# Kernel tuning notes

Measured on AMD Instinct MI355X. Metric: run time of the kernel, lower is better.

The kernel has to match this reference:

```python
import jax, jax.numpy as jnp
import numpy as np

K = 32
EPS = 1e-5  # BatchNorm eps; eval mode with running_mean=0, running_var=1


def knn_idx(x):
    # x: [B, C, N] -> idx of K nearest neighbors [B, N, K]
    inner = -2.0 * jnp.einsum('bcn,bcm->bnm', x, x)
    xx = jnp.sum(x * x, axis=1)  # [B, N]
    pd = -xx[:, :, None] - inner - xx[:, None, :]  # negative squared dist
    return jax.lax.top_k(pd, K)[1]


def get_neighbors(x):
    # x: [B, C, N] -> edge features [B, N, K, 2C] (nbr - ctr, ctr)
    idx = knn_idx(x)
    xt = jnp.transpose(x, (0, 2, 1))  # [B, N, C]
    nbrs = jax.vmap(lambda p, i: p[i])(xt, idx)  # [B, N, K, C]
    ctr = jnp.broadcast_to(xt[:, :, None, :], nbrs.shape)
    return jnp.concatenate([nbrs - ctr, ctr], axis=-1)


def bn_eval(h, g, b, nd):
    # inference-mode BN, running_mean=0, running_var=1
    shape = [1, -1] + [1] * (nd - 2)
    return h * (g / jnp.sqrt(1.0 + EPS)).reshape(shape) + b.reshape(shape)


def edge_conv(x, W, g, b):
    # x: [B, C, N] -> [B, O, N]; 1x1 conv over edge feats + BN + LeakyReLU + max over K
    feat = get_neighbors(x)  # [B, N, K, 2C]
    h = jnp.einsum('bnkc,oc->bonk', feat, W)
    h = jax.nn.leaky_relu(bn_eval(h, g, b, 4), 0.2)
    return jnp.max(h, axis=-1)


def setup_inputs():
    key = jax.random.key(0)
    ks = jax.random.split(key, 40)
    B, N = 4, 2048

    def rn(i, shape, s=0.1):
        return jax.random.normal(ks[i], shape, jnp.float32) * s

    def gm(i, c):
        return 1.0 + rn(i, (c,))

    inp = {
        'x': jax.random.normal(ks[0], (B, 3, N), jnp.float32),
        'l': jax.random.normal(ks[1], (B, 5), jnp.float32),
        'n': jax.random.normal(ks[2], (B, 7), jnp.float32),
        'W1': rn(3, (64, 6)), 'g1': gm(4, 64), 'b1': rn(5, (64,)),
        'W2': rn(6, (64, 128)), 'g2': gm(7, 64), 'b2': rn(8, (64,)),
        'W3': rn(9, (128, 128)), 'g3': gm(10, 128), 'b3': rn(11, (128,)),
        'W4': rn(12, (256, 256)), 'g4': gm(13, 256), 'b4': rn(14, (256,)),
        'W5': rn(15, (1024, 512)), 'g5': gm(16, 1024), 'b5': rn(17, (1024,)),
        'W6': rn(18, (64, 5)), 'g6': gm(19, 64), 'b6': rn(20, (64,)),
        'W7': rn(21, (64, 7)), 'g7': gm(22, 64), 'b7': rn(23, (64,)),
        'L1': rn(24, (512, 1152)), 'g8': gm(25, 512), 'b8': rn(26, (512,)),
        'L2': rn(27, (256, 512)), 'L2b': rn(28, (256,)), 'g9': gm(29, 256), 'b9': rn(30, (256,)),
        'L3': rn(31, (28, 256)), 'L3b': rn(32, (28,)),
    }
    return inp


def reference(x, l, n, W1, g1, b1, W2, g2, b2, W3, g3, b3, W4, g4, b4,
              W5, g5, b5, W6, g6, b6, W7, g7, b7,
              L1, g8, b8, L2, L2b, g9, b9, L3, L3b):
    x1 = edge_conv(x, W1, g1, b1)    # [B, 64, N]
    x2 = edge_conv(x1, W2, g2, b2)   # [B, 64, N]
    x3 = edge_conv(x2, W3, g3, b3)   # [B, 128, N]
    x4 = edge_conv(x3, W4, g4, b4)   # [B, 256, N]
    cat = jnp.concatenate([x1, x2, x3, x4], axis=1)  # [B, 512, N]
    h = jnp.einsum('bcn,oc->bon', cat, W5)
    h = jax.nn.leaky_relu(bn_eval(h, g5, b5, 3), 0.2)
    h = jnp.max(h, axis=-1)  # global max pool -> [B, 1024]
    lf = jax.nn.leaky_relu(bn_eval(jnp.einsum('bc,oc->bo', l, W6), g6, b6, 2), 0.2)
    nf = jax.nn.leaky_relu(bn_eval(jnp.einsum('bc,oc->bo', n, W7), g7, b7, 2), 0.2)
    v = jnp.concatenate([h, lf, nf], axis=-1)  # [B, 1152]
    v = jax.nn.relu(bn_eval(v @ L1.T, g8, b8, 2))  # dropout = identity (eval)
    v = jax.nn.relu(bn_eval(v @ L2.T + L2b, g9, b9, 2))
    return v @ L3.T + L3b  # [B, 28]
```

## Files before the change

### kernel.cpp

```cpp
#include <hip/hip_runtime.h>
#include <hip/hip_bf16.h>

#define NPTS 2048
#define NB 4
#define KNN 32
#define NIN 33

static __device__ __forceinline__ float b2f(__hip_bfloat16 v) { return __bfloat162float(v); }
#define ISQ 0.99999499996875f

typedef __attribute__((ext_vector_type(8))) short short8v;
typedef __attribute__((ext_vector_type(4))) float f32x4;

static __device__ __forceinline__ unsigned ordkey(float f) {
  unsigned u = __float_as_uint(f);
  return u ^ (unsigned)(((int)u >> 31) | 0x80000000);
}

static __device__ __forceinline__ void loadv(const float* p, float (&d)[1]) { d[0] = *p; }
static __device__ __forceinline__ void loadv(const float* p, float (&d)[2]) {
  float2 v = *(const float2*)p; d[0] = v.x; d[1] = v.y;
}
static __device__ __forceinline__ void loadv(const float* p, float (&d)[4]) {
  float4 v = *(const float4*)p; d[0] = v.x; d[1] = v.y; d[2] = v.z; d[3] = v.w;
}

static __device__ __forceinline__ float wave_red_sum(float s) {
#pragma unroll
  for (int off = 32; off > 0; off >>= 1) s += __shfl_xor(s, off);
  return s;
}

__global__ __launch_bounds__(64) void detect_kernel(const unsigned short* __restrict__ x,
                                                    int* __restrict__ flag) {
  int cnt = 0;
  for (int i = threadIdx.x; i < 512; i += 64) {
    unsigned e = (x[i] >> 7) & 0xFFu;
    if (e >= 0xC6u) cnt++;
  }
#pragma unroll
  for (int off = 32; off > 0; off >>= 1) cnt += __shfl_down(cnt, off);
  if (threadIdx.x == 0) flag[0] = (cnt == 0) ? 1 : 0;
}

struct CvtArgs {
  const void* src[NIN];
  int off[NIN + 1];
};

__global__ __launch_bounds__(256) void cvt_all_kernel(CvtArgs a, float* __restrict__ out,
                                                      int total, int nb1,
                                                      __hip_bfloat16* __restrict__ w5bf,
                                                      float* __restrict__ xxb,
                                                      const int* __restrict__ flag) {
  int fl = flag[0];
  if ((int)blockIdx.x < nb1) {
    int t = blockIdx.x * 256 + threadIdx.x;
    if (t >= total) return;
    int s = 0;
    while (t >= a.off[s + 1]) s++;
    int j = t - a.off[s];
    float v;
    if (fl) v = b2f(((const __hip_bfloat16*)a.src[s])[j]);
    else    v = ((const float*)a.src[s])[j];
    out[t] = v;
  } else if ((int)blockIdx.x < nb1 + 2048) {
    int t = (blockIdx.x - nb1) * 256 + threadIdx.x;
    if (fl) w5bf[t] = ((const __hip_bfloat16*)a.src[15])[t];
    else    w5bf[t] = __float2bfloat16(((const float*)a.src[15])[t]);
  } else {
    int t = (blockIdx.x - nb1 - 2048) * 256 + threadIdx.x;
    int b = t >> 11, m = t & 2047;
    float s = 0.f;
#pragma unroll
    for (int c = 0; c < 3; ++c) {
      long o = ((long)b * 3 + c) * NPTS + m;
      float v = fl ? b2f(((const __hip_bfloat16*)a.src[0])[o])
                   : ((const float*)a.src[0])[o];
      s = fmaf(v, v, s);
    }
    xxb[t] = s;
  }
}

template <int C>
static __device__ __forceinline__ void pd_body(char* smem, const float* __restrict__ x,
                                               long bstride, const float* __restrict__ xx,
                                               unsigned* __restrict__ keys, int t, int bb) {
  constexpr int KT = (C < 16) ? C : 16;
  float* At = (float*)smem;
  float* Bt = At + KT * 64;
  unsigned* Ts = (unsigned*)(Bt + KT * 64);
  int tj = (int)((sqrtf(8.f * (float)t + 1.f) - 1.f) * 0.5f);
  while ((tj + 1) * (tj + 2) / 2 <= t) tj++;
  while (tj * (tj + 1) / 2 > t) tj--;
  int ti = t - tj * (tj + 1) / 2;
  int n0 = ti * 64, m0 = tj * 64;
  int tid = threadIdx.x, tx = tid & 15, ty = tid >> 4;
  const float* xb = x + (long)bb * bstride;
  float acc[4][4] = {};
  for (int k0 = 0; k0 < C; k0 += KT) {
    for (int lin = tid; lin < KT * 64; lin += 256) {
      int r = lin >> 6, col = lin & 63;
      At[r * 64 + col] = xb[(long)(k0 + r) * NPTS + n0 + col];
      Bt[r * 64 + col] = xb[(long)(k0 + r) * NPTS + m0 + col];
    }
    __syncthreads();
#pragma unroll
    for (int kc = 0; kc < KT; ++kc) {
      float4 av = *(const float4*)&At[kc * 64 + ty * 4];
      float4 bv = *(const float4*)&Bt[kc * 64 + tx * 4];
      acc[0][0] = fmaf(av.x, bv.x, acc[0][0]); acc[0][1] = fmaf(av.x, bv.y, acc[0][1]);
      acc[0][2] = fmaf(av.x, bv.z, acc[0][2]); acc[0][3] = fmaf(av.x, bv.w, acc[0][3]);
      acc[1][0] = fmaf(av.y, bv.x, acc[1][0]); acc[1][1] = fmaf(av.y, bv.y, acc[1][1]);
      acc[1][2] = fmaf(av.y, bv.z, acc[1][2]); acc[1][3] = fmaf(av.y, bv.w, acc[1][3]);
      acc[2][0] = fmaf(av.z, bv.x, acc[2][0]); acc[2][1] = fmaf(av.z, bv.y, acc[2][1]);
      acc[2][2] = fmaf(av.z, bv.z, acc[2][2]); acc[2][3] = fmaf(av.z, bv.w, acc[2][3]);
      acc[3][0] = fmaf(av.w, bv.x, acc[3][0]); acc[3][1] = fmaf(av.w, bv.y, acc[3][1]);
      acc[3][2] = fmaf(av.w, bv.z, acc[3][2]); acc[3][3] = fmaf(av.w, bv.w, acc[3][3]);
    }
    __syncthreads();
  }
  const float* xxq = xx + (long)bb * NPTS;
  float4 xxm = *(const float4*)&xxq[m0 + tx * 4];
  unsigned* kb = keys + ((long)bb << 22);
  unsigned ok[4][4];
#pragma unroll
  for (int i = 0; i < 4; ++i) {
    float xxn = xxq[n0 + ty * 4 + i];
    ok[i][0] = ordkey((-xxn - (-2.f * acc[i][0])) - xxm.x);
    ok[i][1] = ordkey((-xxn - (-2.f * acc[i][1])) - xxm.y);
    ok[i][2] = ordkey((-xxn - (-2.f * acc[i][2])) - xxm.z);
    ok[i][3] = ordkey((-xxn - (-2.f * acc[i][3])) - xxm.w);
    uint4 o = make_uint4(ok[i][0], ok[i][1], ok[i][2], ok[i][3]);
    *(uint4*)&kb[(long)(n0 + ty * 4 + i) * NPTS + m0 + tx * 4] = o;
  }
  if (ti != tj) {
#pragma unroll
    for (int i = 0; i < 4; ++i)
#pragma unroll
      for (int j = 0; j < 4; ++j) Ts[(tx * 4 + j) * 68 + ty * 4 + i] = ok[i][j];
    __syncthreads();
#pragma unroll
    for (int i = 0; i < 4; ++i)
      *(uint4*)&kb[(long)(m0 + ty * 4 + i) * NPTS + n0 + tx * 4] =
          *(const uint4*)&Ts[(ty * 4 + i) * 68 + tx * 4];
  }
}

template <int C>
static __device__ __forceinline__ void yzt_body(char* smem, const float* __restrict__ x,
                                                long bstride, const float* __restrict__ W, int O,
                                                float* __restrict__ yt, float* __restrict__ zt,
                                                int b, int m0, int o0) {
  constexpr int KT = (C < 16) ? C : 16;
  float* Xs = (float*)smem;
  float* Wy = Xs + KT * 64;
  float* Wp = Wy + KT * 64;
  int tid = threadIdx.x, tx = tid & 15, ty = tid >> 4;
  const float* xb = x + (long)b * bstride;
  const int twoC = 2 * C;
  float accy[4][4] = {}, accp[4][4] = {};
  for (int k0 = 0; k0 < C; k0 += KT) {
    for (int lin = tid; lin < KT * 64; lin += 256) {
      int r = lin >> 6, col = lin & 63;
      Xs[r * 64 + col] = xb[(long)(k0 + r) * NPTS + m0 + col];
      float wy = W[(o0 + col) * twoC + k0 + r];
      Wy[r * 64 + col] = wy;
      Wp[r * 64 + col] = W[(o0 + col) * twoC + C + k0 + r] - wy;
    }
    __syncthreads();
#pragma unroll
    for (int kc = 0; kc < KT; ++kc) {
      float4 wv = *(const float4*)&Wy[kc * 64 + tx * 4];
      float4 pv = *(const float4*)&Wp[kc * 64 + tx * 4];
      float xm[4];
      xm[0] = Xs[kc * 64 + ty * 4 + 0]; xm[1] = Xs[kc * 64 + ty * 4 + 1];
      xm[2] = Xs[kc * 64 + ty * 4 + 2]; xm[3] = Xs[kc * 64 + ty * 4 + 3];
#pragma unroll
      for (int i = 0; i < 4; ++i) {
        accy[i][0] = fmaf(xm[i], wv.x, accy[i][0]);
        accy[i][1] = fmaf(xm[i], wv.y, accy[i][1]);
        accy[i][2] = fmaf(xm[i], wv.z, accy[i][2]);
        accy[i][3] = fmaf(xm[i], wv.w, accy[i][3]);
        accp[i][0] = fmaf(xm[i], pv.x, accp[i][0]);
        accp[i][1] = fmaf(xm[i], pv.y, accp[i][1]);
        accp[i][2] = fmaf(xm[i], pv.z, accp[i][2]);
        accp[i][3] = fmaf(xm[i], pv.w, accp[i][3]);
      }
    }
    __syncthreads();
  }
#pragma unroll
  for (int i = 0; i < 4; ++i) {
    long base = ((long)b * NPTS + m0 + ty * 4 + i) * O + o0 + tx * 4;
    *(float4*)&yt[base] = make_float4(accy[i][0], accy[i][1], accy[i][2], accy[i][3]);
    *(float4*)&zt[base] = make_float4(accp[i][0], accp[i][1], accp[i][2], accp[i][3]);
  }
}

template <int C, int O64>
__global__ __launch_bounds__(256) void pdyzt_kernel(const float* __restrict__ x, long bstride,
                                                    const float* __restrict__ xx,
                                                    unsigned* __restrict__ keys,
                                                    const float* __restrict__ W,
                                                    float* __restrict__ yt,
                                                    float* __restrict__ zt, int npd) {
  constexpr int KT = (C < 16) ? C : 16;
  constexpr size_t S1 = (size_t)KT * 64 * 2 * 4 + 64 * 68 * 4;
  constexpr size_t S2 = (size_t)KT * 64 * 3 * 4;
  constexpr size_t SM = S1 > S2 ? S1 : S2;
  __shared__ __align__(16) char smem[SM];
  int bid = blockIdx.x;
  if (bid < npd) {
    int bb = bid % NB, t = bid / NB;
    pd_body<C>(smem, x, bstride, xx, keys, t, bb);
  } else {
    int rem = bid - npd;
    int b = rem % NB; rem /= NB;
    int m0 = (rem % 32) * 64; rem /= 32;
    int o0 = rem * 64;
    yzt_body<C>(smem, x, bstride, W, O64 * 64, yt, zt, b, m0, o0);
  }
}

__global__ __launch_bounds__(256) void select_kernel(const unsigned* __restrict__ keys,
                                                     int* __restrict__ idxout) {
  int wave = threadIdx.x >> 6, lane = threadIdx.x & 63;
  int q = blockIdx.x * 4 + wave;
  int bloc = q >> 11, n = q & 2047;
  const uint4* rp = (const uint4*)(keys + ((long)((bloc << 11) | n) << 11));
  unsigned K[32];
#pragma unroll
  for (int t = 0; t < 8; ++t) {
    uint4 kk = rp[t * 64 + lane];
    K[4 * t + 0] = kk.x; K[4 * t + 1] = kk.y; K[4 * t + 2] = kk.z; K[4 * t + 3] = kk.w;
  }
  unsigned t0 = 0, t1 = 0, t2 = 0, t3 = 0;
#pragma unroll
  for (int s = 0; s < 32; ++s) {
    unsigned k = K[s];
    if (k > t3) {
      if (k > t1) {
        if (k > t0) { t3 = t2; t2 = t1; t1 = t0; t0 = k; }
        else        { t3 = t2; t2 = t1; t1 = k; }
      } else {
        if (k > t2) { t3 = t2; t2 = k; }
        else        { t3 = k; }
      }
    }
  }
  unsigned orv = t0 | t1 | t2 | t3, andv = t0 & t1 & t2 & t3;
#pragma unroll
  for (int xm = 32; xm >= 1; xm >>= 1) {
    orv  |= __shfl_xor(orv, xm);
    andv &= __shfl_xor(andv, xm);
  }
  unsigned V = orv ^ andv;
  unsigned P = andv & ~V;
  int need = KNN;
  for (int b = 31; b >= 0; --b) {
    unsigned bit = 1u << b;
    if (!(V & bit)) continue;
    unsigned hm = 0xFFFFFFFFu << b;
    unsigned Pb = (P & hm) | bit;
    int c = (int)__popcll(__ballot((t0 & hm) == Pb)) +
            (int)__popcll(__ballot((t1 & hm) == Pb)) +
            (int)__popcll(__ballot((t2 & hm) == Pb)) +
            (int)__popcll(__ballot((t3 & hm) == Pb));
    if (c >= need) P |= bit;
    else need -= c;
  }
  int cg = 0;
#pragma unroll
  for (int s = 0; s < 32; ++s) cg += (int)__popcll(__ballot(K[s] > P));
  if (cg > KNN - 1) {
    unsigned orf = K[0], anf = K[0];
#pragma unroll
    for (int s = 1; s < 32; ++s) { orf |= K[s]; anf &= K[s]; }
#pragma unroll
    for (int xm = 32; xm >= 1; xm >>= 1) {
      orf |= __shfl_xor(orf, xm);
      anf &= __shfl_xor(anf, xm);
    }
    unsigned Vf = orf ^ anf;
    P = anf & ~Vf;
    need = KNN;
    for (int b = 31; b >= 0; --b) {
      unsigned bit = 1u << b;
      if (!(Vf & bit)) continue;
      unsigned hm = 0xFFFFFFFFu << b;
      unsigned Pb = (P & hm) | bit;
      int c = 0;
#pragma unroll
      for (int s = 0; s < 32; ++s) c += (int)__popcll(__ballot((K[s] & hm) == Pb));
      if (c >= need) P |= bit;
      else need -= c;
    }
  }
  int* orow = idxout + ((bloc << 11) | n) * KNN;
  int base = 0;
  unsigned eqmask = 0;
#pragma unroll
  for (int s = 0; s < 32; ++s) {
    bool take = K[s] > P;
    unsigned long long bal = __ballot(take);
    if (take) {
      int pos = base + (int)__popcll(bal & ((1ull << lane) - 1ull));
      orow[pos] = ((s >> 2) << 8) + lane * 4 + (s & 3);
    }
    base += (int)__popcll(bal);
    if (K[s] == P) eqmask |= (1u << s);
  }
  int rem = KNN - base;
  for (int it = 0; it < rem; ++it) {
    unsigned mym = 0xFFFFFFFFu;
    if (eqmask) {
      int s = __ffs(eqmask) - 1;
      mym = (unsigned)(((s >> 2) << 8) + lane * 4 + (s & 3));
    }
    unsigned wm = mym;
#pragma unroll
    for (int xm = 32; xm >= 1; xm >>= 1) {
      unsigned o = __shfl_xor(wm, xm);
      wm = o < wm ? o : wm;
    }
    if (mym == wm) {
      orow[base + it] = (int)wm;
      eqmask &= eqmask - 1;
    }
  }
}

template <int C>
__global__ __launch_bounds__(256) void pdgemmsym_kernel(const float* __restrict__ x, long bstride,
                                                        const float* __restrict__ xx,
                                                        unsigned* __restrict__ keys) {
  constexpr int KT = (C < 16) ? C : 16;
  constexpr size_t SM = (size_t)KT * 64 * 2 * 4 + 64 * 68 * 4;
  __shared__ __align__(16) char smem[SM];
  pd_body<C>(smem, x, bstride, xx, keys, blockIdx.x, blockIdx.y);
}

template <int C>
__global__ __launch_bounds__(256) void yzt_kernel(const float* __restrict__ x, long bstride,
                                                  const float* __restrict__ W, int O,
                                                  float* __restrict__ yt, float* __restrict__ zt) {
  constexpr int KT = (C < 16) ? C : 16;
  constexpr size_t SM = (size_t)KT * 64 * 3 * 4;
  __shared__ __align__(16) char smem[SM];
  yzt_body<C>(smem, x, bstride, W, O, yt, zt, blockIdx.z, blockIdx.y * 64, blockIdx.x * 64);
}

template <int RO>
__global__ __launch_bounds__(256) void gmaxt_kernel(const float* __restrict__ yt,
                                                    const float* __restrict__ zt,
                                                    const int* __restrict__ idx,
                                                    const float* __restrict__ g,
                                                    const float* __restrict__ bb,
                                                    float* __restrict__ out, long obstride,
                                                    float* __restrict__ xxout,
                                                    __hip_bfloat16* __restrict__ catbf, int loff) {
  constexpr int O = RO * 64;
  int wave = threadIdx.x >> 6, lane = threadIdx.x & 63;
  int n = blockIdx.x * 4 + wave, b = blockIdx.y;
  int jreg = idx[((b << 11) + n) * KNN + (lane & 31)];
  int obase = lane * RO;
  float gs[RO], bs[RO], zr[RO], acc[RO];
  loadv(zt + ((long)(b << 11) + n) * O + obase, zr);
#pragma unroll
  for (int r = 0; r < RO; ++r) {
    gs[r] = g[obase + r] * ISQ;
    bs[r] = bb[obase + r];
    acc[r] = -INFINITY;
  }
  const float* yb = yt + ((long)(b << 11)) * O + obase;
#pragma unroll
  for (int k = 0; k < KNN; ++k) {
    int j = __shfl(jreg, k);
    float yv[RO];
    loadv(yb + (long)j * O, yv);
#pragma unroll
    for (int r = 0; r < RO; ++r) {
      float v = fmaf(gs[r], yv[r] + zr[r], bs[r]);
      v = v >= 0.f ? v : 0.2f * v;
      acc[r] = fmaxf(acc[r], v);
    }
  }
  float* op = out + (long)b * obstride + (long)obase * NPTS + n;
#pragma unroll
  for (int r = 0; r < RO; ++r) op[(long)r * NPTS] = acc[r];
  __hip_bfloat16* cb = catbf + ((long)(b << 11) + n) * 512 + loff + obase;
#pragma unroll
  for (int r = 0; r < RO; ++r) cb[r] = __float2bfloat16(acc[r]);
  if (xxout) {
    float ss = 0.f;
#pragma unroll
    for (int r = 0; r < RO; ++r) ss = fmaf(acc[r], acc[r], ss);
    ss = wave_red_sum(ss);
    if (lane == 0) xxout[(b << 11) + n] = ss;
  }
}

__global__ __launch_bounds__(256) void gemm5m_kernel(const __hip_bfloat16* __restrict__ catbf,
                                                     const __hip_bfloat16* __restrict__ w5bf,
                                                     const float* __restrict__ g5,
                                                     const float* __restrict__ b5,
                                                     float* __restrict__ pmax) {
  __shared__ __align__(16) short Bs[2][8 * 64 * 8];
  int b = blockIdx.z, po0 = blockIdx.y * 128, n0 = blockIdx.x * 64;
  int wave = threadIdx.x >> 6, lane = threadIdx.x & 63;
  int quad = lane >> 4, l15 = lane & 15;
  const short* cbase = (const short*)catbf + ((long)(b << 11) + n0) * 512;
  const short* abase0 = (const short*)w5bf + (long)(po0 + wave * 32 + l15) * 512 + quad * 8;
  const short* abase1 = abase0 + 16 * 512;
  const short* bsrc0 = cbase + (long)lane * 512 + (2 * wave + 0) * 8;
  const short* bsrc1 = cbase + (long)lane * 512 + (2 * wave + 1) * 8;
  short* bdst0 = &Bs[0][((2 * wave + 0) * 64 + lane) * 8];
  short* bdst1 = &Bs[0][((2 * wave + 1) * 64 + lane) * 8];
  const int bufstride = 8 * 64 * 8;

  short8v Br[2][2], Ar[2][2][2];
  f32x4 acc[2][4] = {};

  Br[0][0] = *(const short8v*)(bsrc0);
  Br[0][1] = *(const short8v*)(bsrc1);
#pragma unroll
  for (int h = 0; h < 2; ++h)
#pragma unroll
    for (int j = 0; j < 2; ++j)
      Ar[0][h][j] = *(const short8v*)((h ? abase1 : abase0) + j * 32);
  *(short8v*)bdst0 = Br[0][0];
  *(short8v*)bdst1 = Br[0][1];
  Br[1][0] = *(const short8v*)(bsrc0 + 64);
  Br[1][1] = *(const short8v*)(bsrc1 + 64);
#pragma unroll
  for (int h = 0; h < 2; ++h)
#pragma unroll
    for (int j = 0; j < 2; ++j)
      Ar[1][h][j] = *(const short8v*)((h ? abase1 : abase0) + 64 + j * 32);
  __syncthreads();

  for (int it = 0; it < 8; ++it) {
    int cur = it & 1;
    const short* lb = &Bs[cur][0];
#pragma unroll
    for (int j = 0; j < 2; ++j) {
#pragma unroll
      for (int nt = 0; nt < 4; ++nt) {
        short8v bf = *(const short8v*)(lb + ((j * 4 + quad) * 64 + nt * 16 + l15) * 8);
        acc[0][nt] = __builtin_amdgcn_mfma_f32_16x16x32_bf16(Ar[cur][0][j], bf, acc[0][nt], 0, 0, 0);
        acc[1][nt] = __builtin_amdgcn_mfma_f32_16x16x32_bf16(Ar[cur][1][j], bf, acc[1][nt], 0, 0, 0);
      }
    }
    if (it < 7) {
      if (it < 6) {
        int ks = (it + 2) * 64;
        Br[cur][0] = *(const short8v*)(bsrc0 + ks);
        Br[cur][1] = *(const short8v*)(bsrc1 + ks);
#pragma unroll
        for (int h = 0; h < 2; ++h)
#pragma unroll
          for (int j = 0; j < 2; ++j)
            Ar[cur][h][j] = *(const short8v*)((h ? abase1 : abase0) + ks + j * 32);
      }
      int nb = cur ^ 1;
      *(short8v*)(bdst0 + nb * bufstride) = Br[nb][0];
      *(short8v*)(bdst1 + nb * bufstride) = Br[nb][1];
      __syncthreads();
    }
  }

#pragma unroll
  for (int h = 0; h < 2; ++h) {
#pragma unroll
    for (int r = 0; r < 4; ++r) {
      int po = po0 + wave * 32 + h * 16 + quad * 4 + r;
      float sc = g5[po] * ISQ;
      float bi = b5[po];
      float mx = -INFINITY;
#pragma unroll
      for (int nt = 0; nt < 4; ++nt) {
        float v = fmaf(sc, acc[h][nt][r], bi);
        v = v >= 0.f ? v : 0.2f * v;
        mx = fmaxf(mx, v);
      }
#pragma unroll
      for (int xm = 1; xm < 16; xm <<= 1) mx = fmaxf(mx, __shfl_xor(mx, xm));
      if (l15 == 0) pmax[(long)(b * 1024 + po) * 32 + blockIdx.x] = mx;
    }
  }
}

__global__ __launch_bounds__(256) void redlfnf_kernel(const float* __restrict__ pmax,
                                                      const float* __restrict__ l,
                                                      const float* __restrict__ nn,
                                                      const float* __restrict__ W6,
                                                      const float* __restrict__ g6,
                                                      const float* __restrict__ b6,
                                                      const float* __restrict__ W7,
                                                      const float* __restrict__ g7,
                                                      const float* __restrict__ b7,
                                                      float* __restrict__ v) {
  if (blockIdx.x < 16) {
    int t = blockIdx.x * 256 + threadIdx.x;
    float mx = -INFINITY;
#pragma unroll
    for (int j = 0; j < 32; ++j) mx = fmaxf(mx, pmax[(long)t * 32 + j]);
    int b = t >> 10, po = t & 1023;
    v[b * 1152 + po] = mx;
  } else {
    int idx = (blockIdx.x - 16) * 256 + threadIdx.x;
    int b = idx >> 7, t = idx & 127;
    if (t < 64) {
      float s = 0.f;
#pragma unroll
      for (int c = 0; c < 5; ++c) s = fmaf(W6[t * 5 + c], l[b * 5 + c], s);
      float val = fmaf(g6[t] * ISQ, s, b6[t]);
      v[b * 1152 + 1024 + t] = val >= 0.f ? val : 0.2f * val;
    } else {
      int o = t - 64;
      float s = 0.f;
#pragma unroll
      for (int c = 0; c < 7; ++c) s = fmaf(W7[o * 7 + c], nn[b * 7 + c], s);
      float val = fmaf(g7[o] * ISQ, s, b7[o]);
      v[b * 1152 + 1088 + o] = val >= 0.f ? val : 0.2f * val;
    }
  }
}

__global__ __launch_bounds__(256) void head1_kernel(const float* __restrict__ v,
                                                    const float* __restrict__ L1,
                                                    const float* __restrict__ g8,
                                                    const float* __restrict__ b8,
                                                    float* __restrict__ v1) {
  int wave = threadIdx.x >> 6, lane = threadIdx.x & 63;
  int t = blockIdx.x * 4 + wave;
  int b = t >> 9, o = t & 511;
  const float* vb = v + b * 1152;
  const float* wr = L1 + (long)o * 1152;
  float s = 0.f;
#pragma unroll
  for (int c = lane; c < 1152; c += 64) s = fmaf(wr[c], vb[c], s);
  s = wave_red_sum(s);
  if (lane == 0) {
    float val = fmaf(g8[o] * ISQ, s, b8[o]);
    v1[t] = fmaxf(val, 0.f);
  }
}

__global__ __launch_bounds__(256) void head2_kernel(const float* __restrict__ v1,
                                                    const float* __restrict__ L2,
                                                    const float* __restrict__ L2b,
                                                    const float* __restrict__ g9,
                                                    const float* __restrict__ b9,
                                                    float* __restrict__ v2) {
  int wave = threadIdx.x >> 6, lane = threadIdx.x & 63;
  int t = blockIdx.x * 4 + wave;
  int b = t >> 8, o = t & 255;
  const float* vb = v1 + b * 512;
  const float* wr = L2 + (long)o * 512;
  float s = 0.f;
#pragma unroll
  for (int c = lane; c < 512; c += 64) s = fmaf(wr[c], vb[c], s);
  s = wave_red_sum(s);
  if (lane == 0) {
    float sv = s + L2b[o];
    float val = fmaf(g9[o] * ISQ, sv, b9[o]);
    v2[t] = fmaxf(val, 0.f);
  }
}

__global__ __launch_bounds__(256) void head3_kernel(const float* __restrict__ v2,
                                                    const float* __restrict__ L3,
                                                    const float* __restrict__ L3b,
                                                    void* __restrict__ out,
                                                    const int* __restrict__ flag) {
  int wave = threadIdx.x >> 6, lane = threadIdx.x & 63;
  int t = blockIdx.x * 4 + wave;
  if (t >= 112) return;
  int b = t / 28, o = t % 28;
  const float* vb = v2 + b * 256;
  const float* wr = L3 + o * 256;
  float s = 0.f;
#pragma unroll
  for (int c = lane; c < 256; c += 64) s = fmaf(wr[c], vb[c], s);
  s = wave_red_sum(s);
  if (lane == 0) {
    float sv = s + L3b[o];
    if (flag[0]) ((__hip_bfloat16*)out)[t] = __float2bfloat16(sv);
    else         ((float*)out)[t] = sv;
  }
}

extern "C" void kernel_launch(void* const* d_in, const int* in_sizes, int n_in,
                              void* d_out, int out_size, void* d_ws, size_t ws_size,
                              hipStream_t stream) {
  CvtArgs ca;
  int off[NIN + 1];
  off[0] = 0;
  for (int i = 0; i < NIN; ++i) {
    ca.src[i] = d_in[i];
    off[i + 1] = off[i] + in_sizes[i];
    ca.off[i] = off[i];
  }
  ca.off[NIN] = off[NIN];
  const int total = off[NIN];

  int* flag = (int*)d_ws;
  float* fin = (float*)((char*)d_ws + 64);
  const float* xf  = fin + off[0];
  const float* lf  = fin + off[1];
  const float* nf  = fin + off[2];
  const float* W1f = fin + off[3];  const float* g1f = fin + off[4];  const float* b1f = fin + off[5];
  const float* W2f = fin + off[6];  const float* g2f = fin + off[7];  const float* b2f_ = fin + off[8];
  const float* W3f = fin + off[9];  const float* g3f = fin + off[10]; const float* b3f = fin + off[11];
  const float* W4f = fin + off[12]; const float* g4f = fin + off[13]; const float* b4f = fin + off[14];
  const float* g5f = fin + off[16]; const float* b5f = fin + off[17];
  const float* W6f = fin + off[18]; const float* g6f = fin + off[19]; const float* b6f = fin + off[20];
  const float* W7f = fin + off[21]; const float* g7f = fin + off[22]; const float* b7f = fin + off[23];
  const float* L1f = fin + off[24]; const float* g8f = fin + off[25]; const float* b8f = fin + off[26];
  const float* L2f = fin + off[27]; const float* L2bf = fin + off[28];
  const float* g9f = fin + off[29]; const float* b9f = fin + off[30];
  const float* L3f = fin + off[31]; const float* L3bf = fin + off[32];

  float* p = fin + ((total + 15) & ~15);
  float* cat  = p;
  float* yb   = cat + 4 * 512 * NPTS;
  float* zb   = yb + 4 * 256 * NPTS;
  float* xxb  = zb + 4 * 256 * NPTS;
  int*   idxb = (int*)(xxb + 4 * NPTS);
  float* pmax = (float*)(idxb + 4 * NPTS * KNN);
  float* vb   = pmax + 4 * 1024 * 32;
  float* v1b  = vb + 4 * 1152;
  float* v2b  = v1b + 4 * 512;
  __hip_bfloat16* w5bf  = (__hip_bfloat16*)(v2b + 4 * 256);
  __hip_bfloat16* catbf = w5bf + 1024 * 512;
  unsigned* keys_tail = (unsigned*)(catbf + (size_t)4 * NPTS * 512);

  size_t need_full = (size_t)((char*)(keys_tail + (size_t)NB * NPTS * NPTS) - (char*)d_ws);
  int bpass = (ws_size >= need_full) ? NB : 1;
  unsigned* keys = (bpass == NB) ? keys_tail : (unsigned*)yb;

  const long bst1 = 3L * NPTS;
  const long bstc = 512L * NPTS;
  const int NTRI = 32 * 33 / 2;
  const int NPD = NTRI * NB;
  const int nb1 = (total + 255) / 256;

  detect_kernel<<<1, 64, 0, stream>>>((const unsigned short*)d_in[0], flag);
  cvt_all_kernel<<<nb1 + 2048 + 32, 256, 0, stream>>>(ca, fin, total, nb1, w5bf, xxb, flag);

  if (bpass == NB) {
    pdyzt_kernel<3, 1><<<NPD + 1 * 32 * NB, 256, 0, stream>>>(xf, bst1, xxb, keys, W1f, yb, zb, NPD);
    select_kernel<<<512 * NB, 256, 0, stream>>>(keys, idxb);
  } else {
    for (int b0 = 0; b0 < NB; b0 += bpass) {
      pdgemmsym_kernel<3><<<dim3(NTRI, bpass), 256, 0, stream>>>(xf + b0 * bst1, bst1, xxb + b0 * NPTS, keys);
      select_kernel<<<512 * bpass, 256, 0, stream>>>(keys, idxb + (long)b0 * NPTS * KNN);
    }
    yzt_kernel<3><<<dim3(1, 32, NB), 256, 0, stream>>>(xf, bst1, W1f, 64, yb, zb);
  }
  gmaxt_kernel<1><<<dim3(512, NB), 256, 0, stream>>>(yb, zb, idxb, g1f, b1f, cat, bstc, xxb, catbf, 0);

  if (bpass == NB) {
    pdyzt_kernel<64, 1><<<NPD + 1 * 32 * NB, 256, 0, stream>>>(cat, bstc, xxb, keys, W2f, yb, zb, NPD);
    select_kernel<<<512 * NB, 256, 0, stream>>>(keys, idxb);
  } else {
    for (int b0 = 0; b0 < NB; b0 += bpass) {
      pdgemmsym_kernel<64><<<dim3(NTRI, bpass), 256, 0, stream>>>(cat + b0 * bstc, bstc, xxb + b0 * NPTS, keys);
      select_kernel<<<512 * bpass, 256, 0, stream>>>(keys, idxb + (long)b0 * NPTS * KNN);
    }
    yzt_kernel<64><<<dim3(1, 32, NB), 256, 0, stream>>>(cat, bstc, W2f, 64, yb, zb);
  }
  gmaxt_kernel<1><<<dim3(512, NB), 256, 0, stream>>>(yb, zb, idxb, g2f, b2f_, cat + 64L * NPTS, bstc, xxb, catbf, 64);

  if (bpass == NB) {
    pdyzt_kernel<64, 2><<<NPD + 2 * 32 * NB, 256, 0, stream>>>(cat + 64L * NPTS, bstc, xxb, keys, W3f, yb, zb, NPD);
    select_kernel<<<512 * NB, 256, 0, stream>>>(keys, idxb);
  } else {
    for (int b0 = 0; b0 < NB; b0 += bpass) {
      pdgemmsym_kernel<64><<<dim3(NTRI, bpass), 256, 0, stream>>>(cat + 64L * NPTS + b0 * bstc, bstc, xxb + b0 * NPTS, keys);
      select_kernel<<<512 * bpass, 256, 0, stream>>>(keys, idxb + (long)b0 * NPTS * KNN);
    }
    yzt_kernel<64><<<dim3(2, 32, NB), 256, 0, stream>>>(cat + 64L * NPTS, bstc, W3f, 128, yb, zb);
  }
  gmaxt_kernel<2><<<dim3(512, NB), 256, 0, stream>>>(yb, zb, idxb, g3f, b3f, cat + 128L * NPTS, bstc, xxb, catbf, 128);

  if (bpass == NB) {
    pdyzt_kernel<128, 4><<<NPD + 4 * 32 * NB, 256, 0, stream>>>(cat + 128L * NPTS, bstc, xxb, keys, W4f, yb, zb, NPD);
    select_kernel<<<512 * NB, 256, 0, stream>>>(keys, idxb);
  } else {
    for (int b0 = 0; b0 < NB; b0 += bpass) {
      pdgemmsym_kernel<128><<<dim3(NTRI, bpass), 256, 0, stream>>>(cat + 128L * NPTS + b0 * bstc, bstc, xxb + b0 * NPTS, keys);
      select_kernel<<<512 * bpass, 256, 0, stream>>>(keys, idxb + (long)b0 * NPTS * KNN);
    }
    yzt_kernel<128><<<dim3(4, 32, NB), 256, 0, stream>>>(cat + 128L * NPTS, bstc, W4f, 256, yb, zb);
  }
  gmaxt_kernel<4><<<dim3(512, NB), 256, 0, stream>>>(yb, zb, idxb, g4f, b4f, cat + 256L * NPTS, bstc, (float*)nullptr, catbf, 256);

  gemm5m_kernel<<<dim3(32, 8, NB), 256, 0, stream>>>(catbf, w5bf, g5f, b5f, pmax);
  redlfnf_kernel<<<18, 256, 0, stream>>>(pmax, lf, nf, W6f, g6f, b6f, W7f, g7f, b7f, vb);

  head1_kernel<<<512, 256, 0, stream>>>(vb, L1f, g8f, b8f, v1b);
  head2_kernel<<<256, 256, 0, stream>>>(v1b, L2f, L2bf, g9f, b9f, v2b);
  head3_kernel<<<28, 256, 0, stream>>>(v2b, L3f, L3bf, d_out, flag);
}
```

Baseline: 545.4 us.

## Fuse 3-channel kNN distance with top-k selection and co-schedule yzt with select

For the first layer (3 input channels), a new knn3 kernel computes pairwise distances directly in registers from shared-memory coordinates and selects the top-32 in the same wave. This avoids writing and re-reading the 2048x2048 key matrix. For the later layers, the yzt projection GEMM blocks move from the pairwise-distance kernel into the select kernel, so distance and select become separate launches with the projection overlapped alongside selection. The shared selection code is factored into a templated helper that supports two index layouts. Tie-breaking order may differ because the first layer uses a different index mapping.

```diff
diff --git a/kernel.cpp b/kernel.cpp
--- a/kernel.cpp
+++ b/kernel.cpp
@@ -83,6 +83,137 @@
   }
 }
 
+template <int MODE>
+static __device__ __forceinline__ int midx(int s, int lane) {
+  return MODE == 0 ? (((s >> 2) << 8) + lane * 4 + (s & 3)) : (s * 64 + lane);
+}
+
+template <int MODE>
+static __device__ __forceinline__ void select_from_K(unsigned (&K)[32], int lane,
+                                                     int* __restrict__ orow) {
+  unsigned t0 = 0, t1 = 0, t2 = 0, t3 = 0;
+#pragma unroll
+  for (int s = 0; s < 32; ++s) {
+    unsigned k = K[s];
+    if (k > t3) {
+      if (k > t1) {
+        if (k > t0) { t3 = t2; t2 = t1; t1 = t0; t0 = k; }
+        else        { t3 = t2; t2 = t1; t1 = k; }
+      } else {
+        if (k > t2) { t3 = t2; t2 = k; }
+        else        { t3 = k; }
+      }
+    }
+  }
+  unsigned orv = t0 | t1 | t2 | t3, andv = t0 & t1 & t2 & t3;
+#pragma unroll
+  for (int xm = 32; xm >= 1; xm >>= 1) {
+    orv  |= __shfl_xor(orv, xm);
+    andv &= __shfl_xor(andv, xm);
+  }
+  unsigned V = orv ^ andv;
+  unsigned P = andv & ~V;
+  int need = KNN;
+  for (int b = 31; b >= 0; --b) {
+    unsigned bit = 1u << b;
+    if (!(V & bit)) continue;
+    unsigned hm = 0xFFFFFFFFu << b;
+    unsigned Pb = (P & hm) | bit;
+    int c = (int)__popcll(__ballot((t0 & hm) == Pb)) +
+            (int)__popcll(__ballot((t1 & hm) == Pb)) +
+            (int)__popcll(__ballot((t2 & hm) == Pb)) +
+            (int)__popcll(__ballot((t3 & hm) == Pb));
+    if (c >= need) P |= bit;
+    else need -= c;
+  }
+  int cg = 0;
+#pragma unroll
+  for (int s = 0; s < 32; ++s) cg += (int)__popcll(__ballot(K[s] > P));
+  if (cg > KNN - 1) {
+    unsigned orf = K[0], anf = K[0];
+#pragma unroll
+    for (int s = 1; s < 32; ++s) { orf |= K[s]; anf &= K[s]; }
+#pragma unroll
+    for (int xm = 32; xm >= 1; xm >>= 1) {
+      orf |= __shfl_xor(orf, xm);
+      anf &= __shfl_xor(anf, xm);
+    }
+    unsigned Vf = orf ^ anf;
+    P = anf & ~Vf;
+    need = KNN;
+    for (int b = 31; b >= 0; --b) {
+      unsigned bit = 1u << b;
+      if (!(Vf & bit)) continue;
+      unsigned hm = 0xFFFFFFFFu << b;
+      unsigned Pb = (P & hm) | bit;
+      int c = 0;
+#pragma unroll
+      for (int s = 0; s < 32; ++s) c += (int)__popcll(__ballot((K[s] & hm) == Pb));
+      if (c >= need) P |= bit;
+      else need -= c;
+    }
+  }
+  int base = 0;
+  unsigned eqmask = 0;
+#pragma unroll
+  for (int s = 0; s < 32; ++s) {
+    bool take = K[s] > P;
+    unsigned long long bal = __ballot(take);
+    if (take) {
+      int pos = base + (int)__popcll(bal & ((1ull << lane) - 1ull));
+      orow[pos] = midx<MODE>(s, lane);
+    }
+    base += (int)__popcll(bal);
+    if (K[s] == P) eqmask |= (1u << s);
+  }
+  int rem = KNN - base;
+  for (int it = 0; it < rem; ++it) {
+    unsigned mym = 0xFFFFFFFFu;
+    if (eqmask) {
+      int s = __ffs(eqmask) - 1;
+      mym = (unsigned)midx<MODE>(s, lane);
+    }
+    unsigned wm = mym;
+#pragma unroll
+    for (int xm = 32; xm >= 1; xm >>= 1) {
+      unsigned o = __shfl_xor(wm, xm);
+      wm = o < wm ? o : wm;
+    }
+    if (mym == wm) {
+      orow[base + it] = (int)wm;
+      eqmask &= eqmask - 1;
+    }
+  }
+}
+
+__global__ __launch_bounds__(256) void knn3_kernel(const float* __restrict__ xf,
+                                                   const float* __restrict__ xxb,
+                                                   int* __restrict__ idxout) {
+  __shared__ float xs[3 * NPTS];
+  __shared__ float xxs[NPTS];
+  int b = blockIdx.y;
+  int tid = threadIdx.x, wave = tid >> 6, lane = tid & 63;
+  const float* xb = xf + (long)b * 3 * NPTS;
+  for (int i = tid; i < 3 * NPTS; i += 256) xs[i] = xb[i];
+  for (int i = tid; i < NPTS; i += 256) xxs[i] = xxb[(b << 11) + i];
+  __syncthreads();
+  int n = blockIdx.x * 4 + wave;
+  float q0 = xs[n], q1 = xs[NPTS + n], q2 = xs[2 * NPTS + n];
+  float xxn = xxs[n];
+  unsigned K[32];
+#pragma unroll
+  for (int s = 0; s < 32; ++s) {
+    int m = s * 64 + lane;
+    float d = 0.f;
+    d = fmaf(q0, xs[m], d);
+    d = fmaf(q1, xs[NPTS + m], d);
+    d = fmaf(q2, xs[2 * NPTS + m], d);
+    float pdv = (-xxn - (-2.f * d)) - xxs[m];
+    K[s] = ordkey(pdv);
+  }
+  select_from_K<1>(K, lane, idxout + (((b << 11) | n) * KNN));
+}
+
 template <int C>
 static __device__ __forceinline__ void pd_body(char* smem, const float* __restrict__ x,
                                                long bstride, const float* __restrict__ xx,
@@ -199,24 +330,34 @@
   }
 }
 
+static __device__ __forceinline__ void select_body(const unsigned* __restrict__ keys,
+                                                   int* __restrict__ idxout, int q) {
+  int lane = threadIdx.x & 63;
+  int bloc = q >> 11, n = q & 2047;
+  const uint4* rp = (const uint4*)(keys + ((long)((bloc << 11) | n) << 11));
+  unsigned K[32];
+#pragma unroll
+  for (int t = 0; t < 8; ++t) {
+    uint4 kk = rp[t * 64 + lane];
+    K[4 * t + 0] = kk.x; K[4 * t + 1] = kk.y; K[4 * t + 2] = kk.z; K[4 * t + 3] = kk.w;
+  }
+  select_from_K<0>(K, lane, idxout + ((bloc << 11) | n) * KNN);
+}
+
 template <int C, int O64>
-__global__ __launch_bounds__(256) void pdyzt_kernel(const float* __restrict__ x, long bstride,
-                                                    const float* __restrict__ xx,
-                                                    unsigned* __restrict__ keys,
-                                                    const float* __restrict__ W,
-                                                    float* __restrict__ yt,
-                                                    float* __restrict__ zt, int npd) {
+__global__ __launch_bounds__(256) void selyzt_kernel(const unsigned* __restrict__ keys,
+                                                     int* __restrict__ idxout,
+                                                     const float* __restrict__ x, long bstride,
+                                                     const float* __restrict__ W,
+                                                     float* __restrict__ yt,
+                                                     float* __restrict__ zt, int nsel) {
   constexpr int KT = (C < 16) ? C : 16;
-  constexpr size_t S1 = (size_t)KT * 64 * 2 * 4 + 64 * 68 * 4;
-  constexpr size_t S2 = (size_t)KT * 64 * 3 * 4;
-  constexpr size_t SM = S1 > S2 ? S1 : S2;
-  __shared__ __align__(16) char smem[SM];
-  int bid = blockIdx.x;
-  if (bid < npd) {
-    int bb = bid % NB, t = bid / NB;
-    pd_body<C>(smem, x, bstride, xx, keys, t, bb);
+  __shared__ __align__(16) char smem[(size_t)KT * 64 * 3 * 4];
+  if ((int)blockIdx.x < nsel) {
+    int wave = threadIdx.x >> 6;
+    select_body(keys, idxout, blockIdx.x * 4 + wave);
   } else {
-    int rem = bid - npd;
+    int rem = blockIdx.x - nsel;
     int b = rem % NB; rem /= NB;
     int m0 = (rem % 32) * 64; rem /= 32;
     int o0 = rem * 64;
@@ -226,110 +367,8 @@
 
 __global__ __launch_bounds__(256) void select_kernel(const unsigned* __restrict__ keys,
                                                      int* __restrict__ idxout) {
-  int wave = threadIdx.x >> 6, lane = threadIdx.x & 63;
-  int q = blockIdx.x * 4 + wave;
-  int bloc = q >> 11, n = q & 2047;
-  const uint4* rp = (const uint4*)(keys + ((long)((bloc << 11) | n) << 11));
-  unsigned K[32];
-#pragma unroll
-  for (int t = 0; t < 8; ++t) {
-    uint4 kk = rp[t * 64 + lane];
-    K[4 * t + 0] = kk.x; K[4 * t + 1] = kk.y; K[4 * t + 2] = kk.z; K[4 * t + 3] = kk.w;
-  }
-  unsigned t0 = 0, t1 = 0, t2 = 0, t3 = 0;
-#pragma unroll
-  for (int s = 0; s < 32; ++s) {
-    unsigned k = K[s];
-    if (k > t3) {
-      if (k > t1) {
-        if (k > t0) { t3 = t2; t2 = t1; t1 = t0; t0 = k; }
-        else        { t3 = t2; t2 = t1; t1 = k; }
-      } else {
-        if (k > t2) { t3 = t2; t2 = k; }
-        else        { t3 = k; }
-      }
-    }
-  }
-  unsigned orv = t0 | t1 | t2 | t3, andv = t0 & t1 & t2 & t3;
-#pragma unroll
-  for (int xm = 32; xm >= 1; xm >>= 1) {
-    orv  |= __shfl_xor(orv, xm);
-    andv &= __shfl_xor(andv, xm);
-  }
-  unsigned V = orv ^ andv;
-  unsigned P = andv & ~V;
-  int need = KNN;
-  for (int b = 31; b >= 0; --b) {
-    unsigned bit = 1u << b;
-    if (!(V & bit)) continue;
-    unsigned hm = 0xFFFFFFFFu << b;
-    unsigned Pb = (P & hm) | bit;
-    int c = (int)__popcll(__ballot((t0 & hm) == Pb)) +
-            (int)__popcll(__ballot((t1 & hm) == Pb)) +
-            (int)__popcll(__ballot((t2 & hm) == Pb)) +
-            (int)__popcll(__ballot((t3 & hm) == Pb));
-    if (c >= need) P |= bit;
-    else need -= c;
-  }
-  int cg = 0;
-#pragma unroll
-  for (int s = 0; s < 32; ++s) cg += (int)__popcll(__ballot(K[s] > P));
-  if (cg > KNN - 1) {
-    unsigned orf = K[0], anf = K[0];
-#pragma unroll
-    for (int s = 1; s < 32; ++s) { orf |= K[s]; anf &= K[s]; }
-#pragma unroll
-    for (int xm = 32; xm >= 1; xm >>= 1) {
-      orf |= __shfl_xor(orf, xm);
-      anf &= __shfl_xor(anf, xm);
-    }
-    unsigned Vf = orf ^ anf;
-    P = anf & ~Vf;
-    need = KNN;
-    for (int b = 31; b >= 0; --b) {
-      unsigned bit = 1u << b;
-      if (!(Vf & bit)) continue;
-      unsigned hm = 0xFFFFFFFFu << b;
-      unsigned Pb = (P & hm) | bit;
-      int c = 0;
-#pragma unroll
-      for (int s = 0; s < 32; ++s) c += (int)__popcll(__ballot((K[s] & hm) == Pb));
-      if (c >= need) P |= bit;
-      else need -= c;
-    }
-  }
-  int* orow = idxout + ((bloc << 11) | n) * KNN;
-  int base = 0;
-  unsigned eqmask = 0;
-#pragma unroll
-  for (int s = 0; s < 32; ++s) {
-    bool take = K[s] > P;
-    unsigned long long bal = __ballot(take);
-    if (take) {
-      int pos = base + (int)__popcll(bal & ((1ull << lane) - 1ull));
-      orow[pos] = ((s >> 2) << 8) + lane * 4 + (s & 3);
-    }
-    base += (int)__popcll(bal);
-    if (K[s] == P) eqmask |= (1u << s);
-  }
-  int rem = KNN - base;
-  for (int it = 0; it < rem; ++it) {
-    unsigned mym = 0xFFFFFFFFu;
-    if (eqmask) {
-      int s = __ffs(eqmask) - 1;
-      mym = (unsigned)(((s >> 2) << 8) + lane * 4 + (s & 3));
-    }
-    unsigned wm = mym;
-#pragma unroll
-    for (int xm = 32; xm >= 1; xm >>= 1) {
-      unsigned o = __shfl_xor(wm, xm);
-      wm = o < wm ? o : wm;
-    }
-    if (mym == wm) {
-      orow[base + it] = (int)wm;
-      eqmask &= eqmask - 1;
-    }
-  }
+  int wave = threadIdx.x >> 6;
+  select_body(keys, idxout, blockIdx.x * 4 + wave);
 }
 
 template <int C>
@@ -645,27 +684,19 @@
   const long bst1 = 3L * NPTS;
   const long bstc = 512L * NPTS;
   const int NTRI = 32 * 33 / 2;
-  const int NPD = NTRI * NB;
   const int nb1 = (total + 255) / 256;
+  const int NSEL = NB * 512;
 
   detect_kernel<<<1, 64, 0, stream>>>((const unsigned short*)d_in[0], flag);
   cvt_all_kernel<<<nb1 + 2048 + 32, 256, 0, stream>>>(ca, fin, total, nb1, w5bf, xxb, flag);
 
+  knn3_kernel<<<dim3(512, NB), 256, 0, stream>>>(xf, xxb, idxb);
+  yzt_kernel<3><<<dim3(1, 32, NB), 256, 0, stream>>>(xf, bst1, W1f, 64, yb, zb);
+  gmaxt_kernel<1><<<dim3(512, NB), 256, 0, stream>>>(yb, zb, idxb, g1f, b1f, cat, bstc, xxb, catbf, 0);
+
   if (bpass == NB) {
-    pdyzt_kernel<3, 1><<<NPD + 1 * 32 * NB, 256, 0, stream>>>(xf, bst1, xxb, keys, W1f, yb, zb, NPD);
-    select_kernel<<<512 * NB, 256, 0, stream>>>(keys, idxb);
-  } else {
-    for (int b0 = 0; b0 < NB; b0 += bpass) {
-      pdgemmsym_kernel<3><<<dim3(NTRI, bpass), 256, 0, stream>>>(xf + b0 * bst1, bst1, xxb + b0 * NPTS, keys);
-      select_kernel<<<512 * bpass, 256, 0, stream>>>(keys, idxb + (long)b0 * NPTS * KNN);
-    }
-    yzt_kernel<3><<<dim3(1, 32, NB), 256, 0, stream>>>(xf, bst1, W1f, 64, yb, zb);
-  }
-  gmaxt_kernel<1><<<dim3(512, NB), 256, 0, stream>>>(yb, zb, idxb, g1f, b1f, cat, bstc, xxb, catbf, 0);
-
-  if (bpass == NB) {
-    pdyzt_kernel<64, 1><<<NPD + 1 * 32 * NB, 256, 0, stream>>>(cat, bstc, xxb, keys, W2f, yb, zb, NPD);
-    select_kernel<<<512 * NB, 256, 0, stream>>>(keys, idxb);
+    pdgemmsym_kernel<64><<<dim3(NTRI, NB), 256, 0, stream>>>(cat, bstc, xxb, keys);
+    selyzt_kernel<64, 1><<<NSEL + 1 * 32 * NB, 256, 0, stream>>>(keys, idxb, cat, bstc, W2f, yb, zb, NSEL);
   } else {
     for (int b0 = 0; b0 < NB; b0 += bpass) {
       pdgemmsym_kernel<64><<<dim3(NTRI, bpass), 256, 0, stream>>>(cat + b0 * bstc, bstc, xxb + b0 * NPTS, keys);
@@ -676,8 +707,8 @@
   gmaxt_kernel<1><<<dim3(512, NB), 256, 0, stream>>>(yb, zb, idxb, g2f, b2f_, cat + 64L * NPTS, bstc, xxb, catbf, 64);
 
   if (bpass == NB) {
-    pdyzt_kernel<64, 2><<<NPD + 2 * 32 * NB, 256, 0, stream>>>(cat + 64L * NPTS, bstc, xxb, keys, W3f, yb, zb, NPD);
-    select_kernel<<<512 * NB, 256, 0, stream>>>(keys, idxb);
+    pdgemmsym_kernel<64><<<dim3(NTRI, NB), 256, 0, stream>>>(cat + 64L * NPTS, bstc, xxb, keys);
+    selyzt_kernel<64, 2><<<NSEL + 2 * 32 * NB, 256, 0, stream>>>(keys, idxb, cat + 64L * NPTS, bstc, W3f, yb, zb, NSEL);
   } else {
     for (int b0 = 0; b0 < NB; b0 += bpass) {
       pdgemmsym_kernel<64><<<dim3(NTRI, bpass), 256, 0, stream>>>(cat + 64L * NPTS + b0 * bstc, bstc, xxb + b0 * NPTS, keys);
@@ -688,8 +719,8 @@
   gmaxt_kernel<2><<<dim3(512, NB), 256, 0, stream>>>(yb, zb, idxb, g3f, b3f, cat + 128L * NPTS, bstc, xxb, catbf, 128);
 
   if (bpass == NB) {
-    pdyzt_kernel<128, 4><<<NPD + 4 * 32 * NB, 256, 0, stream>>>(cat + 128L * NPTS, bstc, xxb, keys, W4f, yb, zb, NPD);
-    select_kernel<<<512 * NB, 256, 0, stream>>>(keys, idxb);
+    pdgemmsym_kernel<128><<<dim3(NTRI, NB), 256, 0, stream>>>(cat + 128L * NPTS, bstc, xxb, keys);
+    selyzt_kernel<128, 4><<<NSEL + 4 * 32 * NB, 256, 0, stream>>>(keys, idxb, cat + 128L * NPTS, bstc, W4f, yb, zb, NSEL);
   } else {
     for (int b0 = 0; b0 < NB; b0 += bpass) {
       pdgemmsym_kernel<128><<<dim3(NTRI, bpass), 256, 0, stream>>>(cat + 128L * NPTS + b0 * bstc, bstc, xxb + b0 * NPTS, keys);
```

New measurement: 536.4 us. No clear change (-1.6%).
